# Kernel optimization log

Hardware: AMD Instinct MI355X
Metric: run time of the kernel (lower is better)

## Reference

```python
import jax, jax.numpy as jnp
import numpy as np

N_TETS = 200000
IN_FEATURES = 128
OUT_FEATURES = 128
NUM_NEIGHBORS = 4  # NEIGHBORHOOD_SIZE = 5 = self + 4 neighbors


def setup_inputs() -> dict:
    key = jax.random.key(0)
    k1, k2, k3, k4 = jax.random.split(key, 4)
    features = jax.random.normal(k1, (N_TETS, IN_FEATURES), dtype=jnp.float32)
    neighbors = jax.random.randint(k2, (N_TETS, NUM_NEIGHBORS), 0, N_TETS, dtype=jnp.int64)
    # torch nn.Linear convention: W is [out_features, 5*in_features]
    fan_in = (1 + NUM_NEIGHBORS) * IN_FEATURES
    bound = 1.0 / np.sqrt(fan_in)
    W = jax.random.uniform(k3, (OUT_FEATURES, fan_in), minval=-bound, maxval=bound, dtype=jnp.float32)
    b = jax.random.uniform(k4, (OUT_FEATURES,), minval=-bound, maxval=bound, dtype=jnp.float32)
    return {"features": features, "neighbors": neighbors, "W": W, "b": b}


def reference(features, neighbors, W, b):
    # Gather neighbor features: [N, 4, F]
    nbr_feats = features[neighbors]
    N = features.shape[0]
    # Concat self + 4 neighbors along feature dim -> [N, 5F]
    stacked = jnp.concatenate([features[:, None, :], nbr_feats], axis=1).reshape(N, -1)
    # Linear + ReLU (torch: x @ W.T + b)
    return jax.nn.relu(stacked @ W.T + b)
```

## Files before the change

### kernel.cpp

```cpp
#include <hip/hip_runtime.h>
#include <stdint.h>

#define NTETS   200000
#define FEATS   128
#define OUTF    128
#define NG      5
#define BM      128
#define NTHR    512
#define NBLOCKS ((NTETS + BM - 1) / BM)

typedef __attribute__((ext_vector_type(8))) short  short8v;
typedef __attribute__((ext_vector_type(4))) float  f32x4;

static __device__ __forceinline__ unsigned short bf16_rne(float f) {
  union { float f; unsigned u; } v; v.f = f;
  unsigned r = v.u + 0x7FFFu + ((v.u >> 16) & 1u);
  return (unsigned short)(r >> 16);
}

static __device__ __forceinline__ void gload_lds16(const void* g, void* l) {
  __builtin_amdgcn_global_load_lds(
      (const __attribute__((address_space(1))) unsigned int*)g,
      (__attribute__((address_space(3))) unsigned int*)l, 16, 0, 0);
}

__global__ void detect_mode_k(const int* __restrict__ nbr, int* __restrict__ flag) {
  int t = threadIdx.x;
  int nz = 0;
  for (int i = t; i < 4096; i += 64) nz |= nbr[2 * i + 1];
  unsigned long long any = __ballot(nz != 0);
  if (t == 0) flag[0] = (any == 0ULL) ? 1 : 0;
}

__global__ void prep_wfrag_k(const float* __restrict__ W, unsigned short* __restrict__ wf) {
  int id = blockIdx.x * 256 + threadIdx.x;
  if (id >= NG * 16384) return;
  int e  = id & 7;
  int l6 = (id >> 3) & 63;
  int ns = (id >> 9) & 7;
  int kk = (id >> 12) & 3;
  int g  = id >> 14;
  int n = ns * 16 + (l6 & 15);
  int k = g * 128 + kk * 32 + (l6 >> 4) * 8 + e;
  wf[id] = bf16_rne(W[n * (NG * FEATS) + k]);
}

__global__ __launch_bounds__(256) void prep_f_k(const float* __restrict__ feat,
                                                unsigned short* __restrict__ fimg) {
  size_t i = ((size_t)blockIdx.x * 256 + threadIdx.x) * 8;
  f32x4 a = *(const f32x4*)(feat + i);
  f32x4 b = *(const f32x4*)(feat + i + 4);
  short8v v;
  v[0] = (short)bf16_rne(a[0]); v[1] = (short)bf16_rne(a[1]);
  v[2] = (short)bf16_rne(a[2]); v[3] = (short)bf16_rne(a[3]);
  v[4] = (short)bf16_rne(b[0]); v[5] = (short)bf16_rne(b[1]);
  v[6] = (short)bf16_rne(b[2]); v[7] = (short)bf16_rne(b[3]);
  *(short8v*)(fimg + i) = v;
}

__global__ __launch_bounds__(NTHR, 4) void conv_k(
    const unsigned short* __restrict__ fimg, const int* __restrict__ nbr,
    const float* __restrict__ bias, const unsigned short* __restrict__ wf,
    const int* __restrict__ mode, float* __restrict__ out)
{
  __shared__ __align__(16) char wtile[2][32768];
  __shared__ unsigned srcoff[NG][BM];

  const int t    = threadIdx.x;
  const int row0 = blockIdx.x * BM;
  const int lane = t & 63;
  const int wv   = t >> 6;
  const int lr   = lane & 15;
  const int lk   = lane >> 4;

  {
    const bool m64 = (mode[0] != 0);
    for (int e = t; e < NG * BM; e += NTHR) {
      int g = e >> 7, r = e & (BM - 1);
      int gr = row0 + r;
      int s = 0;
      if (gr < NTETS) {
        if (g == 0) s = gr;
        else {
          size_t idx = (size_t)gr * 4 + (g - 1);
          s = m64 ? nbr[2 * idx] : nbr[idx];
          if ((unsigned)s >= (unsigned)NTETS) s = 0;
        }
      }
      srcoff[g][r] = (unsigned)s * 256u;
    }
  }
  __syncthreads();

  const char* fimgc = (const char*)fimg;
  unsigned aoff[NG];
#pragma unroll
  for (int g = 0; g < NG; ++g)
    aoff[g] = srcoff[g][wv * 16 + lr] + (unsigned)(lk * 16);

  const f32x4 zero = {0.f, 0.f, 0.f, 0.f};
  f32x4 acc[8];
#pragma unroll
  for (int i = 0; i < 8; ++i) acc[i] = zero;

  short8v a[2][4];

#define SB() __builtin_amdgcn_sched_barrier(0)

#define A_ISSUE(gg) do {                                                        \
    _Pragma("unroll")                                                           \
    for (int kk_ = 0; kk_ < 4; ++kk_)                                           \
      a[(gg) & 1][kk_] = *(const short8v*)(fimgc + aoff[gg] + kk_ * 64);        \
  } while (0)

#define W_ISSUE(gg) do {                                                        \
    const char* ws_ = (const char*)wf + (gg) * 32768 + wv * 4096 + (lane << 4); \
    _Pragma("unroll")                                                           \
    for (int i_ = 0; i_ < 4; ++i_)                                              \
      gload_lds16(ws_ + i_ * 1024, &wtile[(gg) & 1][wv * 4096 + i_ * 1024]);    \
  } while (0)

  A_ISSUE(0); SB();
  W_ISSUE(0); SB();
  W_ISSUE(1); SB();
  asm volatile("s_waitcnt vmcnt(4)" ::: "memory");
  SB();
  __builtin_amdgcn_s_barrier();

#pragma unroll
  for (int g = 0; g < NG; ++g) {
    const int bi = g & 1;
    if (g + 1 < NG) { A_ISSUE(g + 1); }
    SB();
#pragma unroll
    for (int kk = 0; kk < 4; ++kk) {
      short8v b[8];
#pragma unroll
      for (int ns = 0; ns < 8; ++ns)
        b[ns] = *(const short8v*)(&wtile[bi][(kk * 8 + ns) * 1024 + (lane << 4)]);
      if (kk == 3 && g + 2 < NG) {
        asm volatile("s_waitcnt lgkmcnt(0)" ::: "memory");
        SB();
        __builtin_amdgcn_s_barrier();
        W_ISSUE(g + 2);
        SB();
      }
#pragma unroll
      for (int ns = 0; ns < 8; ++ns)
        acc[ns] = __builtin_amdgcn_mfma_f32_16x16x32_bf16(a[bi][kk], b[ns], acc[ns], 0, 0, 0);
    }
    SB();
    if (g <= 2) {
      asm volatile("s_waitcnt vmcnt(8)" ::: "memory");
      SB();
      __builtin_amdgcn_s_barrier();
    } else if (g == 3) {
      asm volatile("s_waitcnt vmcnt(4)" ::: "memory");
      SB();
      __builtin_amdgcn_s_barrier();
    }
  }

#pragma unroll
  for (int ns = 0; ns < 8; ++ns) {
    const int col = ns * 16 + lr;
    const float bv = bias[col];
    const int rbase = row0 + wv * 16 + lk * 4;
#pragma unroll
    for (int i = 0; i < 4; ++i) {
      int r = rbase + i;
      if (r < NTETS) {
        float vv = acc[ns][i] + bv;
        out[(size_t)r * OUTF + col] = vv > 0.f ? vv : 0.f;
      }
    }
  }
#undef A_ISSUE
#undef W_ISSUE
#undef SB
}

extern "C" void kernel_launch(void* const* d_in, const int* in_sizes, int n_in,
                              void* d_out, int out_size, void* d_ws, size_t ws_size,
                              hipStream_t stream) {
  const float* feat = (const float*)d_in[0];
  const int*   nbr  = (const int*)d_in[1];
  const float* W    = (const float*)d_in[2];
  const float* bias = (const float*)d_in[3];
  float* out = (float*)d_out;

  int* mode = (int*)d_ws;
  unsigned short* wf   = (unsigned short*)((char*)d_ws + 1024);
  unsigned short* fimg = (unsigned short*)((char*)d_ws + 164864);

  detect_mode_k<<<1, 64, 0, stream>>>(nbr, mode);
  prep_wfrag_k<<<320, 256, 0, stream>>>(W, wf);
  prep_f_k<<<(NTETS * FEATS / 8 + 255) / 256, 256, 0, stream>>>(feat, fimg);
  conv_k<<<NBLOCKS, NTHR, 0, stream>>>(fimg, nbr, bias, wf, mode, out);
}
```

Measured before the change: 116.7 us.

## Use 3-stage half-group pipeline with smaller LDS tiles and nontemporal I/O

Splits each 128-wide K group into two 64-wide sub-steps and streams weights through a triple-buffered 16KB LDS ring instead of a double-buffered 32KB one. This cuts LDS per block and raises the occupancy hint from 4 to 6 blocks per CU. It also drops the mid-loop lgkmcnt wait and barrier so global loads overlap with MFMA. The feature-conversion loads and output stores become nontemporal to reduce cache pollution. Waiting on vmcnt at finer granularity adds a barrier every sub-step, and the higher occupancy target may cause register spills.

```diff
diff --git a/kernel.cpp b/kernel.cpp
--- a/kernel.cpp
+++ b/kernel.cpp
@@ -8,6 +8,8 @@
 #define BM      128
 #define NTHR    512
 #define NBLOCKS ((NTETS + BM - 1) / BM)
+#define SUBS    10
+#define SUBW    16384
 
 typedef __attribute__((ext_vector_type(8))) short  short8v;
 typedef __attribute__((ext_vector_type(4))) float  f32x4;
@@ -48,8 +50,8 @@
 __global__ __launch_bounds__(256) void prep_f_k(const float* __restrict__ feat,
                                                 unsigned short* __restrict__ fimg) {
   size_t i = ((size_t)blockIdx.x * 256 + threadIdx.x) * 8;
-  f32x4 a = *(const f32x4*)(feat + i);
-  f32x4 b = *(const f32x4*)(feat + i + 4);
+  f32x4 a = __builtin_nontemporal_load((const f32x4*)(feat + i));
+  f32x4 b = __builtin_nontemporal_load((const f32x4*)(feat + i + 4));
   short8v v;
   v[0] = (short)bf16_rne(a[0]); v[1] = (short)bf16_rne(a[1]);
   v[2] = (short)bf16_rne(a[2]); v[3] = (short)bf16_rne(a[3]);
@@ -58,12 +60,12 @@
   *(short8v*)(fimg + i) = v;
 }
 
-__global__ __launch_bounds__(NTHR, 4) void conv_k(
+__global__ __launch_bounds__(NTHR, 6) void conv_k(
     const unsigned short* __restrict__ fimg, const int* __restrict__ nbr,
     const float* __restrict__ bias, const unsigned short* __restrict__ wf,
     const int* __restrict__ mode, float* __restrict__ out)
 {
-  __shared__ __align__(16) char wtile[2][32768];
+  __shared__ __align__(16) char wtile[3][SUBW];
   __shared__ unsigned srcoff[NG][BM];
 
   const int t    = threadIdx.x;
@@ -103,59 +105,58 @@
 #pragma unroll
   for (int i = 0; i < 8; ++i) acc[i] = zero;
 
-  short8v a[2][4];
+  short8v a[3][2];
 
 #define SB() __builtin_amdgcn_sched_barrier(0)
 
-#define A_ISSUE(gg) do {                                                        \
-    _Pragma("unroll")                                                           \
-    for (int kk_ = 0; kk_ < 4; ++kk_)                                           \
-      a[(gg) & 1][kk_] = *(const short8v*)(fimgc + aoff[gg] + kk_ * 64);        \
+#define A_ISSUE(ss) do {                                                          \
+    a[(ss) % 3][0] = *(const short8v*)(fimgc + aoff[(ss) >> 1] +                  \
+                                       (((ss) & 1) * 2 + 0) * 64);                \
+    a[(ss) % 3][1] = *(const short8v*)(fimgc + aoff[(ss) >> 1] +                  \
+                                       (((ss) & 1) * 2 + 1) * 64);                \
   } while (0)
 
-#define W_ISSUE(gg) do {                                                        \
-    const char* ws_ = (const char*)wf + (gg) * 32768 + wv * 4096 + (lane << 4); \
-    _Pragma("unroll")                                                           \
-    for (int i_ = 0; i_ < 4; ++i_)                                              \
-      gload_lds16(ws_ + i_ * 1024, &wtile[(gg) & 1][wv * 4096 + i_ * 1024]);    \
+#define W_ISSUE(ss) do {                                                          \
+    const char* ws_ = (const char*)wf + (size_t)(ss) * SUBW + wv * 2048 +         \
+                      (lane << 4);                                                \
+    char* wd_ = &wtile[(ss) % 3][wv * 2048];                                      \
+    gload_lds16(ws_, wd_);                                                        \
+    gload_lds16(ws_ + 1024, wd_ + 1024);                                          \
   } while (0)
 
+  W_ISSUE(0); SB();
   A_ISSUE(0); SB();
-  W_ISSUE(0); SB();
   W_ISSUE(1); SB();
+  A_ISSUE(1); SB();
   asm volatile("s_waitcnt vmcnt(4)" ::: "memory");
   SB();
   __builtin_amdgcn_s_barrier();
 
 #pragma unroll
-  for (int g = 0; g < NG; ++g) {
-    const int bi = g & 1;
-    if (g + 1 < NG) { A_ISSUE(g + 1); }
+  for (int s = 0; s < SUBS; ++s) {
+    if (s + 2 < SUBS) {
+      W_ISSUE(s + 2); SB();
+      A_ISSUE(s + 2); SB();
+    }
+    {
+      short8v b[8];
+#pragma unroll
+      for (int ns = 0; ns < 8; ++ns)
+        b[ns] = *(const short8v*)(&wtile[s % 3][ns * 1024 + (lane << 4)]);
+#pragma unroll
+      for (int ns = 0; ns < 8; ++ns)
+        acc[ns] = __builtin_amdgcn_mfma_f32_16x16x32_bf16(a[s % 3][0], b[ns], acc[ns], 0, 0, 0);
+#pragma unroll
+      for (int ns = 0; ns < 8; ++ns)
+        b[ns] = *(const short8v*)(&wtile[s % 3][(8 + ns) * 1024 + (lane << 4)]);
+#pragma unroll
+      for (int ns = 0; ns < 8; ++ns)
+        acc[ns] = __builtin_amdgcn_mfma_f32_16x16x32_bf16(a[s % 3][1], b[ns], acc[ns], 0, 0, 0);
+    }
     SB();
-#pragma unroll
-    for (int kk = 0; kk < 4; ++kk) {
-      short8v b[8];
-#pragma unroll
-      for (int ns = 0; ns < 8; ++ns)
-        b[ns] = *(const short8v*)(&wtile[bi][(kk * 8 + ns) * 1024 + (lane << 4)]);
-      if (kk == 3 && g + 2 < NG) {
-        asm volatile("s_waitcnt lgkmcnt(0)" ::: "memory");
-        SB();
-        __builtin_amdgcn_s_barrier();
-        W_ISSUE(g + 2);
-        SB();
-      }
-#pragma unroll
-      for (int ns = 0; ns < 8; ++ns)
-        acc[ns] = __builtin_amdgcn_mfma_f32_16x16x32_bf16(a[bi][kk], b[ns], acc[ns], 0, 0, 0);
-    }
-    SB();
-    if (g <= 2) {
-      asm volatile("s_waitcnt vmcnt(8)" ::: "memory");
-      SB();
-      __builtin_amdgcn_s_barrier();
-    } else if (g == 3) {
-      asm volatile("s_waitcnt vmcnt(4)" ::: "memory");
+    if (s + 1 < SUBS) {
+      if (s + 2 < SUBS) asm volatile("s_waitcnt vmcnt(4)" ::: "memory");
+      else              asm volatile("s_waitcnt vmcnt(0)" ::: "memory");
       SB();
       __builtin_amdgcn_s_barrier();
     }
@@ -171,7 +172,8 @@
       int r = rbase + i;
       if (r < NTETS) {
         float vv = acc[ns][i] + bv;
-        out[(size_t)r * OUTF + col] = vv > 0.f ? vv : 0.f;
+        vv = vv > 0.f ? vv : 0.f;
+        __builtin_nontemporal_store(vv, &out[(size_t)r * OUTF + col]);
       }
     }
   }
```

Result: faster. 111.4 us (-4.5%).
